# Optimization experiments

Hardware: AMD Instinct MI355X
Metric: run time of the kernel (lower is better)

Reference implementation:

```python
import jax, jax.numpy as jnp
import numpy as np

B, S, E, KD = 4, 4096, 128, 64

def setup_inputs() -> dict:
    key = jax.random.key(0)
    k1, k2, k3, k4 = jax.random.split(key, 4)
    x = jax.random.normal(k1, (B, S, E), dtype=jnp.float32)
    Wk = jax.random.normal(k2, (KD, E), dtype=jnp.float32) * (1.0 / np.sqrt(E))
    Wq = jax.random.normal(k3, (KD, E), dtype=jnp.float32) * (1.0 / np.sqrt(E))
    Wv = jax.random.normal(k4, (E, E), dtype=jnp.float32) * (1.0 / np.sqrt(E))
    return {"x": x, "Wk": Wk, "Wq": Wq, "Wv": Wv}

def reference(x, Wk, Wq, Wv):
    # x: [B, S, E]; torch Linear(weight [out,in], no bias) -> x @ W.T
    key = jnp.einsum('bse,ke->bsk', x, Wk)      # [B, S, KD]
    query = jnp.einsum('bse,ke->bsk', x, Wq)    # [B, S, KD]
    value = jnp.einsum('bse,ve->bsv', x, Wv)    # [B, S, E]
    # NOTE: faithful to original: tril applied to K^T ([B, KD, S]),
    # i.e. element (d, s) of K^T kept only if s <= d (NOT a causal score mask).
    kT_masked = jnp.tril(jnp.swapaxes(key, 1, 2))  # [B, KD, S]
    scores = jnp.einsum('bsk,bkt->bst', query, kT_masked)  # [B, S, S]
    scores = jax.nn.softmax(scores, axis=2)
    return jnp.einsum('bst,btv->bsv', scores, value)  # [B, S, E]
```

## Files before the change

### kernel.cpp

```cpp
#include <hip/hip_runtime.h>

#define BB 4
#define SS 4096
#define EE 128

typedef __attribute__((ext_vector_type(8))) short bf16x8;
typedef __attribute__((ext_vector_type(4))) float f32x4;

__device__ __forceinline__ unsigned short f2bf(float f) {
    unsigned u = __float_as_uint(f);
    u = (u + 0x7FFFu + ((u >> 16) & 1u)) >> 16;
    return (unsigned short)u;
}
__device__ __forceinline__ float bf2f(unsigned short h) {
    return __uint_as_float(((unsigned)h) << 16);
}
__device__ __forceinline__ void split8(const float* p, bf16x8& h, bf16x8& l) {
    float4 v0 = *reinterpret_cast<const float4*>(p);
    float4 v1 = *reinterpret_cast<const float4*>(p + 4);
    float f[8] = {v0.x, v0.y, v0.z, v0.w, v1.x, v1.y, v1.z, v1.w};
    #pragma unroll
    for (int i = 0; i < 8; ++i) {
        unsigned short hb = f2bf(f[i]);
        h[i] = (short)hb;
        l[i] = (short)f2bf(f[i] - bf2f(hb));
    }
}

__global__ __launch_bounds__(256, 2)
void prep(const float* __restrict__ x, const float* __restrict__ Wk,
          const float* __restrict__ Wq, const float* __restrict__ Wv,
          unsigned short* __restrict__ Vt,
          unsigned short* __restrict__ Mth, unsigned short* __restrict__ Mtl,
          float* __restrict__ vpart)
{
    __shared__ float xs[64][132];
    __shared__ float wst[128][68];
    const int tid = threadIdx.x;
    const int bx = blockIdx.x;

    if (bx < 256) {
        float* w = &wst[0][0];
        const int b = bx >> 6, i = bx & 63;
        const size_t base = ((size_t)b * SS + 64 + (size_t)i * 63) * EE;
        const int col = tid & 127, rg = tid >> 7;
        float s = 0.f;
        for (int r = rg; r < 63; r += 2)
            s += x[base + (size_t)r * EE + col];
        w[rg * 128 + col] = s;
        __syncthreads();
        if (tid < 128) w[256 + tid] = w[tid] + w[128 + tid];
        __syncthreads();
        if (tid < 128) {
            float a = 0.f;
            #pragma unroll 8
            for (int e = 0; e < 128; e += 4) {
                float4 wv = *reinterpret_cast<const float4*>(Wv + (size_t)tid * EE + e);
                a = fmaf(w[256 + e + 0], wv.x, a);
                a = fmaf(w[256 + e + 1], wv.y, a);
                a = fmaf(w[256 + e + 2], wv.z, a);
                a = fmaf(w[256 + e + 3], wv.w, a);
            }
            vpart[((size_t)b * 64 + i) * 128 + tid] = a;
        }
        return;
    }

    const int idx = bx - 256;
    const int b = idx / 3, role = idx % 3;
    const size_t xrow0 = (size_t)b * SS;
    const float* Wbase = (role == 0) ? Wv : (role == 1) ? (Wv + 64 * EE) : Wk;

    #pragma unroll
    for (int i = 0; i < 8; ++i) {
        int f4 = tid + i * 256;
        int row = f4 >> 5, kq = f4 & 31;
        float4 v = *reinterpret_cast<const float4*>(x + (xrow0 + row) * EE + 4 * kq);
        *reinterpret_cast<float4*>(&xs[row][4 * kq]) = v;
    }
    #pragma unroll
    for (int i = 0; i < 8; ++i) {
        int f4 = tid + i * 256;
        int c = f4 & 63, kq = f4 >> 6;
        float4 v = *reinterpret_cast<const float4*>(Wbase + (size_t)c * EE + 4 * kq);
        wst[4 * kq + 0][c] = v.x;
        wst[4 * kq + 1][c] = v.y;
        wst[4 * kq + 2][c] = v.z;
        wst[4 * kq + 3][c] = v.w;
    }
    __syncthreads();

    const int ct = tid & 15, rt = tid >> 4;
    const int c0 = 4 * ct, r0 = 4 * rt;
    float acc[4][4] = {};
    #pragma unroll 4
    for (int k0 = 0; k0 < 128; k0 += 4) {
        float4 a[4], bq[4];
        #pragma unroll
        for (int i = 0; i < 4; ++i) a[i] = *reinterpret_cast<const float4*>(&xs[r0 + i][k0]);
        #pragma unroll
        for (int kk = 0; kk < 4; ++kk) bq[kk] = *reinterpret_cast<const float4*>(&wst[k0 + kk][c0]);
        #pragma unroll
        for (int i = 0; i < 4; ++i) {
            const float4 ai = a[i];
            acc[i][0] = fmaf(ai.x, bq[0].x, acc[i][0]);
            acc[i][1] = fmaf(ai.x, bq[0].y, acc[i][1]);
            acc[i][2] = fmaf(ai.x, bq[0].z, acc[i][2]);
            acc[i][3] = fmaf(ai.x, bq[0].w, acc[i][3]);
            acc[i][0] = fmaf(ai.y, bq[1].x, acc[i][0]);
            acc[i][1] = fmaf(ai.y, bq[1].y, acc[i][1]);
            acc[i][2] = fmaf(ai.y, bq[1].z, acc[i][2]);
            acc[i][3] = fmaf(ai.y, bq[1].w, acc[i][3]);
            acc[i][0] = fmaf(ai.z, bq[2].x, acc[i][0]);
            acc[i][1] = fmaf(ai.z, bq[2].y, acc[i][1]);
            acc[i][2] = fmaf(ai.z, bq[2].z, acc[i][2]);
            acc[i][3] = fmaf(ai.z, bq[2].w, acc[i][3]);
            acc[i][0] = fmaf(ai.w, bq[3].x, acc[i][0]);
            acc[i][1] = fmaf(ai.w, bq[3].y, acc[i][1]);
            acc[i][2] = fmaf(ai.w, bq[3].z, acc[i][2]);
            acc[i][3] = fmaf(ai.w, bq[3].w, acc[i][3]);
        }
    }

    if (role <= 1) {
        const int voff = role * 64;
        #pragma unroll
        for (int j = 0; j < 4; ++j) {
            ushort4 pk = make_ushort4(f2bf(acc[0][j]), f2bf(acc[1][j]),
                                      f2bf(acc[2][j]), f2bf(acc[3][j]));
            *reinterpret_cast<ushort4*>(Vt + (size_t)b * 8192 + (size_t)(voff + c0 + j) * 64 + r0) = pk;
        }
        return;
    }

    __syncthreads();
    float (*ks)[68] = reinterpret_cast<float (*)[68]>(&wst[0][0]);
    #pragma unroll
    for (int i = 0; i < 4; ++i)
        #pragma unroll
        for (int j = 0; j < 4; ++j) {
            const int t = r0 + i, k = c0 + j;
            ks[k][t] = (t <= k) ? acc[i][j] : 0.f;
        }
    #pragma unroll
    for (int i = 0; i < 8; ++i) {
        int f4 = tid + i * 256;
        int row = f4 >> 5, kq = f4 & 31;
        float4 v = *reinterpret_cast<const float4*>(Wq + (size_t)row * EE + 4 * kq);
        *reinterpret_cast<float4*>(&xs[row][4 * kq]) = v;
    }
    __syncthreads();

    const int tt = tid >> 5, te = tid & 31;
    const int t0 = tt * 8, e0 = te * 4;
    float a2[8][4] = {};
    #pragma unroll 8
    for (int j = 0; j < 64; ++j) {
        float4 wq = *reinterpret_cast<const float4*>(&xs[j][e0]);
        float4 ka = *reinterpret_cast<const float4*>(&ks[j][t0]);
        float4 kb = *reinterpret_cast<const float4*>(&ks[j][t0 + 4]);
        float kv[8] = {ka.x, ka.y, ka.z, ka.w, kb.x, kb.y, kb.z, kb.w};
        #pragma unroll
        for (int i = 0; i < 8; ++i) {
            a2[i][0] = fmaf(kv[i], wq.x, a2[i][0]);
            a2[i][1] = fmaf(kv[i], wq.y, a2[i][1]);
            a2[i][2] = fmaf(kv[i], wq.z, a2[i][2]);
            a2[i][3] = fmaf(kv[i], wq.w, a2[i][3]);
        }
    }
    #pragma unroll
    for (int i = 0; i < 8; ++i) {
        unsigned short h0 = f2bf(a2[i][0]), h1 = f2bf(a2[i][1]);
        unsigned short h2 = f2bf(a2[i][2]), h3 = f2bf(a2[i][3]);
        ushort4 hv = make_ushort4(h0, h1, h2, h3);
        ushort4 lv = make_ushort4(f2bf(a2[i][0] - bf2f(h0)),
                                  f2bf(a2[i][1] - bf2f(h1)),
                                  f2bf(a2[i][2] - bf2f(h2)),
                                  f2bf(a2[i][3] - bf2f(h3)));
        const size_t off = (size_t)b * 8192 + (size_t)(t0 + i) * 128 + e0;
        *reinterpret_cast<ushort4*>(Mth + off) = hv;
        *reinterpret_cast<ushort4*>(Mtl + off) = lv;
    }
}

__global__ __launch_bounds__(64)
void attn_main(const float* __restrict__ x, const short* __restrict__ Mth,
               const short* __restrict__ Mtl, const short* __restrict__ Vt,
               const float* __restrict__ vpart, float* __restrict__ out)
{
    __shared__ float Plds[16][68];
    __shared__ float vsS[128];
    const int l = threadIdx.x;
    const int b = blockIdx.y;
    const int s0 = blockIdx.x * 16;
    const int lm = l & 15, lg = l >> 4;

    float2 vac = make_float2(0.f, 0.f);
    {
        const float* vp = vpart + (size_t)b * 8192 + 2 * l;
        #pragma unroll 8
        for (int i = 0; i < 64; ++i) {
            float2 t = *reinterpret_cast<const float2*>(vp + (size_t)i * 128);
            vac.x += t.x; vac.y += t.y;
        }
    }
    *reinterpret_cast<float2*>(&vsS[2 * l]) = vac;

    bf16x8 xh[4], xl[4];
    const float* xrow = x + ((size_t)b * SS + s0 + lm) * EE + lg * 8;
    #pragma unroll
    for (int kt = 0; kt < 4; ++kt)
        split8(xrow + kt * 32, xh[kt], xl[kt]);

    f32x4 sa[4];
    const short* mh_base = Mth + (size_t)b * 8192 + lg * 8;
    const short* ml_base = Mtl + (size_t)b * 8192 + lg * 8;
    #pragma unroll
    for (int ct = 0; ct < 4; ++ct) {
        f32x4 a = {0.f, 0.f, 0.f, 0.f};
        const size_t trow = (size_t)(ct * 16 + lm) * 128;
        #pragma unroll
        for (int kt = 0; kt < 4; ++kt) {
            bf16x8 mh = *reinterpret_cast<const bf16x8*>(mh_base + trow + kt * 32);
            bf16x8 ml = *reinterpret_cast<const bf16x8*>(ml_base + trow + kt * 32);
            a = __builtin_amdgcn_mfma_f32_16x16x32_bf16(xh[kt], mh, a, 0, 0, 0);
            a = __builtin_amdgcn_mfma_f32_16x16x32_bf16(xl[kt], mh, a, 0, 0, 0);
            a = __builtin_amdgcn_mfma_f32_16x16x32_bf16(xh[kt], ml, a, 0, 0, 0);
        }
        sa[ct] = a;
    }

    float e[4], iz[4];
    #pragma unroll
    for (int r = 0; r < 4; ++r) {
        float m = fmaxf(fmaxf(sa[0][r], sa[1][r]), fmaxf(sa[2][r], sa[3][r]));
        #pragma unroll
        for (int o = 1; o < 16; o <<= 1) m = fmaxf(m, __shfl_xor(m, o));
        m = fmaxf(m, 0.f);
        float w0 = __expf(sa[0][r] - m), w1 = __expf(sa[1][r] - m);
        float w2 = __expf(sa[2][r] - m), w3 = __expf(sa[3][r] - m);
        sa[0][r] = w0; sa[1][r] = w1; sa[2][r] = w2; sa[3][r] = w3;
        float z = (w0 + w1) + (w2 + w3);
        #pragma unroll
        for (int o = 1; o < 16; o <<= 1) z += __shfl_xor(z, o);
        e[r] = __expf(-m);
        z += 4032.f * e[r];
        iz[r] = 1.f / z;
    }

    #pragma unroll
    for (int ct = 0; ct < 4; ++ct)
        #pragma unroll
        for (int r = 0; r < 4; ++r)
            Plds[lg * 4 + r][ct * 16 + lm] = sa[ct][r];
    bf16x8 pf[2];
    #pragma unroll
    for (int kt2 = 0; kt2 < 2; ++kt2) {
        const float* pr = &Plds[lm][kt2 * 32 + lg * 8];
        #pragma unroll
        for (int i = 0; i < 8; ++i) pf[kt2][i] = (short)f2bf(pr[i]);
    }

    const short* vb = Vt + (size_t)b * 8192 + lg * 8;
    const size_t obase = ((size_t)b * SS + s0) * EE;
    #pragma unroll
    for (int ct = 0; ct < 8; ++ct) {
        const int col = ct * 16 + lm;
        bf16x8 v0 = *reinterpret_cast<const bf16x8*>(vb + (size_t)col * 64);
        bf16x8 v1 = *reinterpret_cast<const bf16x8*>(vb + (size_t)col * 64 + 32);
        f32x4 a = {0.f, 0.f, 0.f, 0.f};
        a = __builtin_amdgcn_mfma_f32_16x16x32_bf16(pf[0], v0, a, 0, 0, 0);
        a = __builtin_amdgcn_mfma_f32_16x16x32_bf16(pf[1], v1, a, 0, 0, 0);
        const float vs = vsS[col];
        #pragma unroll
        for (int r = 0; r < 4; ++r)
            out[obase + (size_t)(lg * 4 + r) * EE + col] = (a[r] + e[r] * vs) * iz[r];
    }
}

extern "C" void kernel_launch(void* const* d_in, const int* in_sizes, int n_in,
                              void* d_out, int out_size, void* d_ws, size_t ws_size,
                              hipStream_t stream)
{
    const float* x  = (const float*)d_in[0];
    const float* Wk = (const float*)d_in[1];
    const float* Wq = (const float*)d_in[2];
    const float* Wv = (const float*)d_in[3];
    float* out = (float*)d_out;

    float* ws = (float*)d_ws;
    float* vpart = ws;
    unsigned short* Mth = (unsigned short*)(vpart + 32768);
    unsigned short* Mtl = Mth + 32768;
    unsigned short* Vt  = Mtl + 32768;

    prep<<<268, 256, 0, stream>>>(x, Wk, Wq, Wv, Vt, Mth, Mtl, vpart);
    attn_main<<<dim3(SS / 16, BB), 64, 0, stream>>>(
        x, (const short*)Mth, (const short*)Mtl, (const short*)Vt, vpart, out);
}
```

Before: 31.15 us.

## Compute prep projections with split-bf16 MFMA in one block per batch

```diff
diff --git a/kernel.cpp b/kernel.cpp
--- a/kernel.cpp
+++ b/kernel.cpp
@@ -25,6 +25,12 @@
         h[i] = (short)hb;
         l[i] = (short)f2bf(f[i] - bf2f(hb));
     }
+}
+__device__ __forceinline__ f32x4 mfma3(bf16x8 ah, bf16x8 al, bf16x8 bh, bf16x8 bl, f32x4 c) {
+    c = __builtin_amdgcn_mfma_f32_16x16x32_bf16(ah, bh, c, 0, 0, 0);
+    c = __builtin_amdgcn_mfma_f32_16x16x32_bf16(al, bh, c, 0, 0, 0);
+    c = __builtin_amdgcn_mfma_f32_16x16x32_bf16(ah, bl, c, 0, 0, 0);
+    return c;
 }
 
 __global__ __launch_bounds__(256, 2)
@@ -34,13 +40,14 @@
           unsigned short* __restrict__ Mth, unsigned short* __restrict__ Mtl,
           float* __restrict__ vpart)
 {
-    __shared__ float xs[64][132];
-    __shared__ float wst[128][68];
+    __shared__ unsigned short wqTh[128][72];
+    __shared__ unsigned short wqTl[128][72];
+    __shared__ float ksub[64][68];
     const int tid = threadIdx.x;
     const int bx = blockIdx.x;
 
     if (bx < 256) {
-        float* w = &wst[0][0];
+        float* w = &ksub[0][0];
         const int b = bx >> 6, i = bx & 63;
         const size_t base = ((size_t)b * SS + 64 + (size_t)i * 63) * EE;
         const int col = tid & 127, rg = tid >> 7;
@@ -66,120 +73,90 @@
         return;
     }
 
-    const int idx = bx - 256;
-    const int b = idx / 3, role = idx % 3;
-    const size_t xrow0 = (size_t)b * SS;
-    const float* Wbase = (role == 0) ? Wv : (role == 1) ? (Wv + 64 * EE) : Wk;
+    const int b = bx - 256;
+    const int l = tid & 63, wv_ = tid >> 6;
+    const int lm = l & 15, lg = l >> 4;
+    const int t0 = wv_ * 16;
 
     #pragma unroll
     for (int i = 0; i < 8; ++i) {
         int f4 = tid + i * 256;
-        int row = f4 >> 5, kq = f4 & 31;
-        float4 v = *reinterpret_cast<const float4*>(x + (xrow0 + row) * EE + 4 * kq);
-        *reinterpret_cast<float4*>(&xs[row][4 * kq]) = v;
-    }
-    #pragma unroll
-    for (int i = 0; i < 8; ++i) {
-        int f4 = tid + i * 256;
-        int c = f4 & 63, kq = f4 >> 6;
-        float4 v = *reinterpret_cast<const float4*>(Wbase + (size_t)c * EE + 4 * kq);
-        wst[4 * kq + 0][c] = v.x;
-        wst[4 * kq + 1][c] = v.y;
-        wst[4 * kq + 2][c] = v.z;
-        wst[4 * kq + 3][c] = v.w;
+        int j = f4 >> 5, eq = f4 & 31;
+        float4 v = *reinterpret_cast<const float4*>(Wq + (size_t)j * EE + 4 * eq);
+        float vf[4] = {v.x, v.y, v.z, v.w};
+        #pragma unroll
+        for (int c = 0; c < 4; ++c) {
+            unsigned short hb = f2bf(vf[c]);
+            wqTh[4 * eq + c][j] = hb;
+            wqTl[4 * eq + c][j] = f2bf(vf[c] - bf2f(hb));
+        }
+    }
+
+    bf16x8 xh[4], xl[4];
+    const float* xrow = x + ((size_t)b * SS + t0 + lm) * EE + lg * 8;
+    #pragma unroll
+    for (int kt = 0; kt < 4; ++kt)
+        split8(xrow + kt * 32, xh[kt], xl[kt]);
+
+    #pragma unroll
+    for (int jt = 0; jt < 4; ++jt) {
+        f32x4 a = {0.f, 0.f, 0.f, 0.f};
+        const float* wkr = Wk + (size_t)(jt * 16 + lm) * EE + lg * 8;
+        #pragma unroll
+        for (int kt = 0; kt < 4; ++kt) {
+            bf16x8 bh, bl;
+            split8(wkr + kt * 32, bh, bl);
+            a = mfma3(xh[kt], xl[kt], bh, bl, a);
+        }
+        const int j = jt * 16 + lm;
+        #pragma unroll
+        for (int r = 0; r < 4; ++r) {
+            const int t = t0 + lg * 4 + r;
+            ksub[t][j] = (t <= j) ? a[r] : 0.f;
+        }
     }
     __syncthreads();
 
-    const int ct = tid & 15, rt = tid >> 4;
-    const int c0 = 4 * ct, r0 = 4 * rt;
-    float acc[4][4] = {};
-    #pragma unroll 4
-    for (int k0 = 0; k0 < 128; k0 += 4) {
-        float4 a[4], bq[4];
-        #pragma unroll
-        for (int i = 0; i < 4; ++i) a[i] = *reinterpret_cast<const float4*>(&xs[r0 + i][k0]);
-        #pragma unroll
-        for (int kk = 0; kk < 4; ++kk) bq[kk] = *reinterpret_cast<const float4*>(&wst[k0 + kk][c0]);
-        #pragma unroll
-        for (int i = 0; i < 4; ++i) {
-            const float4 ai = a[i];
-            acc[i][0] = fmaf(ai.x, bq[0].x, acc[i][0]);
-            acc[i][1] = fmaf(ai.x, bq[0].y, acc[i][1]);
-            acc[i][2] = fmaf(ai.x, bq[0].z, acc[i][2]);
-            acc[i][3] = fmaf(ai.x, bq[0].w, acc[i][3]);
-            acc[i][0] = fmaf(ai.y, bq[1].x, acc[i][0]);
-            acc[i][1] = fmaf(ai.y, bq[1].y, acc[i][1]);
-            acc[i][2] = fmaf(ai.y, bq[1].z, acc[i][2]);
-            acc[i][3] = fmaf(ai.y, bq[1].w, acc[i][3]);
-            acc[i][0] = fmaf(ai.z, bq[2].x, acc[i][0]);
-            acc[i][1] = fmaf(ai.z, bq[2].y, acc[i][1]);
-            acc[i][2] = fmaf(ai.z, bq[2].z, acc[i][2]);
-            acc[i][3] = fmaf(ai.z, bq[2].w, acc[i][3]);
-            acc[i][0] = fmaf(ai.w, bq[3].x, acc[i][0]);
-            acc[i][1] = fmaf(ai.w, bq[3].y, acc[i][1]);
-            acc[i][2] = fmaf(ai.w, bq[3].z, acc[i][2]);
-            acc[i][3] = fmaf(ai.w, bq[3].w, acc[i][3]);
-        }
-    }
-
-    if (role <= 1) {
-        const int voff = role * 64;
-        #pragma unroll
-        for (int j = 0; j < 4; ++j) {
-            ushort4 pk = make_ushort4(f2bf(acc[0][j]), f2bf(acc[1][j]),
-                                      f2bf(acc[2][j]), f2bf(acc[3][j]));
-            *reinterpret_cast<ushort4*>(Vt + (size_t)b * 8192 + (size_t)(voff + c0 + j) * 64 + r0) = pk;
-        }
-        return;
-    }
-
-    __syncthreads();
-    float (*ks)[68] = reinterpret_cast<float (*)[68]>(&wst[0][0]);
-    #pragma unroll
-    for (int i = 0; i < 4; ++i)
-        #pragma unroll
-        for (int j = 0; j < 4; ++j) {
-            const int t = r0 + i, k = c0 + j;
-            ks[k][t] = (t <= k) ? acc[i][j] : 0.f;
-        }
-    #pragma unroll
-    for (int i = 0; i < 8; ++i) {
-        int f4 = tid + i * 256;
-        int row = f4 >> 5, kq = f4 & 31;
-        float4 v = *reinterpret_cast<const float4*>(Wq + (size_t)row * EE + 4 * kq);
-        *reinterpret_cast<float4*>(&xs[row][4 * kq]) = v;
-    }
-    __syncthreads();
-
-    const int tt = tid >> 5, te = tid & 31;
-    const int t0 = tt * 8, e0 = te * 4;
-    float a2[8][4] = {};
-    #pragma unroll 8
-    for (int j = 0; j < 64; ++j) {
-        float4 wq = *reinterpret_cast<const float4*>(&xs[j][e0]);
-        float4 ka = *reinterpret_cast<const float4*>(&ks[j][t0]);
-        float4 kb = *reinterpret_cast<const float4*>(&ks[j][t0 + 4]);
-        float kv[8] = {ka.x, ka.y, ka.z, ka.w, kb.x, kb.y, kb.z, kb.w};
-        #pragma unroll
-        for (int i = 0; i < 8; ++i) {
-            a2[i][0] = fmaf(kv[i], wq.x, a2[i][0]);
-            a2[i][1] = fmaf(kv[i], wq.y, a2[i][1]);
-            a2[i][2] = fmaf(kv[i], wq.z, a2[i][2]);
-            a2[i][3] = fmaf(kv[i], wq.w, a2[i][3]);
-        }
-    }
-    #pragma unroll
-    for (int i = 0; i < 8; ++i) {
-        unsigned short h0 = f2bf(a2[i][0]), h1 = f2bf(a2[i][1]);
-        unsigned short h2 = f2bf(a2[i][2]), h3 = f2bf(a2[i][3]);
-        ushort4 hv = make_ushort4(h0, h1, h2, h3);
-        ushort4 lv = make_ushort4(f2bf(a2[i][0] - bf2f(h0)),
-                                  f2bf(a2[i][1] - bf2f(h1)),
-                                  f2bf(a2[i][2] - bf2f(h2)),
-                                  f2bf(a2[i][3] - bf2f(h3)));
-        const size_t off = (size_t)b * 8192 + (size_t)(t0 + i) * 128 + e0;
-        *reinterpret_cast<ushort4*>(Mth + off) = hv;
-        *reinterpret_cast<ushort4*>(Mtl + off) = lv;
+    bf16x8 kh[2], kl[2];
+    #pragma unroll
+    for (int kt2 = 0; kt2 < 2; ++kt2)
+        split8(&ksub[t0 + lm][kt2 * 32 + lg * 8], kh[kt2], kl[kt2]);
+    #pragma unroll
+    for (int et = 0; et < 8; ++et) {
+        f32x4 a = {0.f, 0.f, 0.f, 0.f};
+        #pragma unroll
+        for (int kt2 = 0; kt2 < 2; ++kt2) {
+            const int e = et * 16 + lm, j0 = kt2 * 32 + lg * 8;
+            bf16x8 qh = *reinterpret_cast<const bf16x8*>(&wqTh[e][j0]);
+            bf16x8 ql = *reinterpret_cast<const bf16x8*>(&wqTl[e][j0]);
+            a = mfma3(kh[kt2], kl[kt2], qh, ql, a);
+        }
+        #pragma unroll
+        for (int r = 0; r < 4; ++r) {
+            const int t = t0 + lg * 4 + r, e = et * 16 + lm;
+            const size_t off = (size_t)b * 8192 + (size_t)t * 128 + e;
+            unsigned short hb = f2bf(a[r]);
+            Mth[off] = hb;
+            Mtl[off] = f2bf(a[r] - bf2f(hb));
+        }
+    }
+
+    #pragma unroll
+    for (int vt = 0; vt < 8; ++vt) {
+        f32x4 a = {0.f, 0.f, 0.f, 0.f};
+        const float* wvr = Wv + (size_t)(vt * 16 + lm) * EE + lg * 8;
+        #pragma unroll
+        for (int kt = 0; kt < 4; ++kt) {
+            bf16x8 bh, bl;
+            split8(wvr + kt * 32, bh, bl);
+            a = mfma3(xh[kt], xl[kt], bh, bl, a);
+        }
+        const int v = vt * 16 + lm;
+        #pragma unroll
+        for (int r = 0; r < 4; ++r) {
+            const int t = t0 + lg * 4 + r;
+            Vt[(size_t)b * 8192 + (size_t)v * 64 + t] = f2bf(a[r]);
+        }
     }
 }
 
@@ -294,7 +271,7 @@
     unsigned short* Mtl = Mth + 32768;
     unsigned short* Vt  = Mtl + 32768;
 
-    prep<<<268, 256, 0, stream>>>(x, Wk, Wq, Wv, Vt, Mth, Mtl, vpart);
+    prep<<<260, 256, 0, stream>>>(x, Wk, Wq, Wv, Vt, Mth, Mtl, vpart);
     attn_main<<<dim3(SS / 16, BB), 64, 0, stream>>>(
         x, (const short*)Mth, (const short*)Mtl, (const short*)Vt, vpart, out);
 }
```

New measurement: 37.46 us. 20.3% more time.
